# Optimization experiments

Measured on AMD Instinct MI355X. Metric: run time of the kernel, lower is better.

## Reference

```python
import jax, jax.numpy as jnp
import numpy as np

B, N, S = 4, 4096, 1024
C1, C2, CO, K = 128, 256, 128, 16
BN_EPS = 1e-5


def setup_inputs() -> dict:
    key = jax.random.key(0)
    ks = jax.random.split(key, 8)
    s = 0.05
    return {
        "xyz1": jax.random.normal(ks[0], (B, N, 3), jnp.float32),
        "xyz2": jax.random.normal(ks[1], (B, S, 3), jnp.float32),
        "points1": jax.random.normal(ks[2], (B, C1, N), jnp.float32),
        "points2": jax.random.normal(ks[3], (B, C2, S), jnp.float32),
        # fuse = ConvBNReLU1D(384 -> 128, k=1)
        "fuse_w": jax.random.normal(ks[4], (CO, C1 + C2), jnp.float32) * s,
        "fuse_b": jnp.zeros((CO,), jnp.float32),
        "fuse_gamma": jnp.ones((CO,), jnp.float32),
        "fuse_beta": jnp.zeros((CO,), jnp.float32),
        # LaplacianUnit conv1x1 (128 -> 128) + BN
        "lu_w": jax.random.normal(ks[5], (CO, CO), jnp.float32) * s,
        "lu_b": jnp.zeros((CO,), jnp.float32),
        "lu_gamma": jnp.ones((CO,), jnp.float32),
        "lu_beta": jnp.zeros((CO,), jnp.float32),
    }


def _sqdist(a, b):
    # a: [B,N,3], b: [B,M,3] -> [B,N,M] squared euclidean distance
    return ((a * a).sum(-1)[:, :, None] + (b * b).sum(-1)[:, None, :]
            - 2.0 * jnp.einsum("bnc,bmc->bnm", a, b))


def _batchnorm1d(x, gamma, beta):
    # x: [B,C,N], training-mode BN (batch statistics, biased variance)
    mean = x.mean(axis=(0, 2), keepdims=True)
    var = ((x - mean) ** 2).mean(axis=(0, 2), keepdims=True)
    xn = (x - mean) * jax.lax.rsqrt(var + BN_EPS)
    return xn * gamma[None, :, None] + beta[None, :, None]


def _gather_points(pts, idx):
    # pts: [B,M,C], idx: [B,N,k] int -> [B,N,k,C]
    return jax.vmap(lambda p, i: p[i])(pts, idx)


def _forward(xyz1, xyz2, points1, points2,
             fuse_w, fuse_b, fuse_gamma, fuse_beta,
             lu_w, lu_b, lu_gamma, lu_beta):
    p2 = jnp.swapaxes(points2, 1, 2)  # [B,S,C2]
    # --- 3-point interpolation (note: torch code uses topk default largest=True) ---
    dists = _sqdist(xyz1, xyz2)                    # [B,N,S]
    top_d, idx = jax.lax.top_k(dists, 3)           # largest, descending (faithful)
    dist_recip = 1.0 / (top_d + 1e-8)
    weight = dist_recip / dist_recip.sum(axis=2, keepdims=True)  # [B,N,3]
    interp = (_gather_points(p2, idx) * weight[..., None]).sum(axis=2)  # [B,N,C2]
    # --- concat skip + fuse conv1x1 + BN + ReLU ---
    new_pts = jnp.concatenate([jnp.swapaxes(points1, 1, 2), interp], axis=-1)  # [B,N,C1+C2]
    x = jnp.einsum("oc,bnc->bon", fuse_w, new_pts) + fuse_b[None, :, None]     # [B,CO,N]
    x = jax.nn.relu(_batchnorm1d(x, fuse_gamma, fuse_beta))
    # --- LaplacianUnit: KNN(k=16) neighbor-sum minus self ---
    d_self = _sqdist(xyz1, xyz1)                   # [B,N,N]
    _, knn_idx = jax.lax.top_k(-d_self, K)         # k smallest distances -> [B,N,K]
    xt = jnp.swapaxes(x, 1, 2)                     # [B,N,CO]
    nbr_sum = _gather_points(xt, knn_idx).sum(axis=2)  # [B,N,CO]
    dx = jnp.swapaxes(nbr_sum, 1, 2) - x           # [B,CO,N]
    h = jnp.einsum("oc,bcn->bon", lu_w, dx) + lu_b[None, :, None]
    h = _batchnorm1d(jax.nn.relu(h), lu_gamma, lu_beta)  # bn(relu(conv(dx))), faithful order
    return x + h


def reference(xyz1, xyz2, points1, points2,
              fuse_w, fuse_b, fuse_gamma, fuse_beta,
              lu_w, lu_b, lu_gamma, lu_beta):
    return _forward(xyz1, xyz2, points1, points2,
                    fuse_w, fuse_b, fuse_gamma, fuse_beta,
                    lu_w, lu_b, lu_gamma, lu_beta)
```

## Files before the change

kernel.cpp:

```cpp
#include <hip/hip_runtime.h>
#include <cfloat>

#define NB 4
#define NN 4096
#define NS 1024
#define NC1 128
#define NC2 256
#define NCO 128
#define NCC 384
#define NK 16
#define KCHUNK 2048
#define KCAP 160
#define KPAD 161


__device__ __forceinline__ float norm3_np(float x, float y, float z) {
  return __fadd_rn(__fadd_rn(__fmul_rn(x, x), __fmul_rn(y, y)), __fmul_rn(z, z));
}

__device__ __forceinline__ float sqdist_np(float nq, float ns,
                                           float qx, float qy, float qz,
                                           float sx, float sy, float sz) {
  float dot = __fadd_rn(__fadd_rn(__fmul_rn(qx, sx), __fmul_rn(qy, sy)),
                        __fmul_rn(qz, sz));
  return __fsub_rn(__fadd_rn(nq, ns), __fmul_rn(2.0f, dot));
}

__global__ void transpose_k(const float* __restrict__ in, float* __restrict__ out,
                            int rows_in, int cols_in, long in_bs, long out_bs, int out_rs) {
  __shared__ float tile[32][33];
  const int b = blockIdx.z;
  const int c0 = blockIdx.x * 32, r0 = blockIdx.y * 32;
  const float* ib = in + (long)b * in_bs;
  float* ob = out + (long)b * out_bs;
#pragma unroll
  for (int k = 0; k < 32; k += 8) {
    tile[threadIdx.y + k][threadIdx.x] =
        ib[(long)(r0 + threadIdx.y + k) * cols_in + c0 + threadIdx.x];
  }
  __syncthreads();
#pragma unroll
  for (int k = 0; k < 32; k += 8) {
    ob[(long)(c0 + threadIdx.y + k) * out_rs + (r0 + threadIdx.x)] =
        tile[threadIdx.x][threadIdx.y + k];
  }
}

__global__ __launch_bounds__(256) void interp_top3_k(const float* __restrict__ xyz1,
                                                     const float* __restrict__ xyz2,
                                                     float* __restrict__ wW,
                                                     int* __restrict__ wIdx) {
  __shared__ float sx[NS], sy[NS], sz[NS], sn[NS];
  __shared__ float md[256 * 3];
  __shared__ int mi[256 * 3];
  const int b = blockIdx.y;
  const int tid = threadIdx.x;
  for (int i = tid; i < NS; i += 256) {
    long base = ((long)b * NS + i) * 3;
    float x = xyz2[base], y = xyz2[base + 1], z = xyz2[base + 2];
    sx[i] = x; sy[i] = y; sz[i] = z;
    sn[i] = norm3_np(x, y, z);
  }
  __syncthreads();
  const int q = (blockIdx.x << 5) + (tid >> 3);
  const int lane = tid & 7;
  long qb = ((long)b * NN + q) * 3;
  const float qx = xyz1[qb], qy = xyz1[qb + 1], qz = xyz1[qb + 2];
  const float nq = norm3_np(qx, qy, qz);
  float bd[3] = {-FLT_MAX, -FLT_MAX, -FLT_MAX};
  int bi[3] = {0x7fffffff, 0x7fffffff, 0x7fffffff};
  for (int s = lane; s < NS; s += 8) {
    float d = sqdist_np(nq, sn[s], qx, qy, qz, sx[s], sy[s], sz[s]);
    float cd = d; int ci = s;
#pragma unroll
    for (int j = 0; j < 3; ++j) {
      bool gt = cd > bd[j];
      float f = fmaxf(cd, bd[j]);
      float bk = fminf(cd, bd[j]);
      int fi = gt ? ci : bi[j];
      int ki = gt ? bi[j] : ci;
      bd[j] = f; bi[j] = fi; cd = bk; ci = ki;
    }
  }
#pragma unroll
  for (int j = 0; j < 3; ++j) { md[tid * 3 + j] = bd[j]; mi[tid * 3 + j] = bi[j]; }
  __syncthreads();
  if (lane == 0) {
    int p0 = 0, p1 = 0, p2 = 0, p3 = 0, p4 = 0, p5 = 0, p6 = 0, p7 = 0;
    float od[3]; int oi[3];
#pragma unroll
    for (int j = 0; j < 3; ++j) {
      float bv = -FLT_MAX; int bidx = 0x7fffffff; int bl = 0;
#define ITOP_CAND(l, pl)                                                     \
      {                                                                      \
        float t = (pl < 3) ? md[(tid + l) * 3 + pl] : -FLT_MAX;              \
        int ti = (pl < 3) ? mi[(tid + l) * 3 + pl] : 0x7fffffff;             \
        if (t > bv || (t == bv && ti < bidx)) { bv = t; bidx = ti; bl = l; } \
      }
      ITOP_CAND(0, p0) ITOP_CAND(1, p1) ITOP_CAND(2, p2) ITOP_CAND(3, p3)
      ITOP_CAND(4, p4) ITOP_CAND(5, p5) ITOP_CAND(6, p6) ITOP_CAND(7, p7)
#undef ITOP_CAND
      od[j] = bv; oi[j] = bidx;
      p0 += (bl == 0); p1 += (bl == 1); p2 += (bl == 2); p3 += (bl == 3);
      p4 += (bl == 4); p5 += (bl == 5); p6 += (bl == 6); p7 += (bl == 7);
    }
    float r0 = 1.f / (od[0] + 1e-8f);
    float r1 = 1.f / (od[1] + 1e-8f);
    float r2 = 1.f / (od[2] + 1e-8f);
    float sR = __fadd_rn(__fadd_rn(r0, r1), r2);
    long obase = ((long)b * NN + q) * 3;
    wW[obase + 0] = r0 / sR; wW[obase + 1] = r1 / sR; wW[obase + 2] = r2 / sR;
    wIdx[obase + 0] = oi[0]; wIdx[obase + 1] = oi[1]; wIdx[obase + 2] = oi[2];
  }
}

__global__ __launch_bounds__(256) void interp_fill_k(const float* __restrict__ p2t,
                                                     const float* __restrict__ wW,
                                                     const int* __restrict__ wIdx,
                                                     float* __restrict__ nt) {
  const int q = (blockIdx.x << 1) + (threadIdx.x >> 7);
  const int co = threadIdx.x & 127;
  const int b = q >> 12;
  long wb = (long)q * 3;
  float w0 = wW[wb], w1 = wW[wb + 1], w2 = wW[wb + 2];
  int i0 = wIdx[wb], i1 = wIdx[wb + 1], i2 = wIdx[wb + 2];
  const float* r0 = p2t + ((long)(b << 10) + i0) * NC2;
  const float* r1 = p2t + ((long)(b << 10) + i1) * NC2;
  const float* r2 = p2t + ((long)(b << 10) + i2) * NC2;
  float* orow = nt + (long)q * NCC + NC1;
#pragma unroll
  for (int h = 0; h < 2; ++h) {
    int c = co + 128 * h;
    orow[c] = w0 * r0[c] + w1 * r1[c] + w2 * r2[c];
  }
}

template <int C>
__global__ __launch_bounds__(256) void gemm_bias_k(const float* __restrict__ feat,
                                                   const float* __restrict__ W,
                                                   const float* __restrict__ bias,
                                                   float* __restrict__ out) {
  __shared__ float fL[64][36];
  __shared__ float wL[64][36];
  const int r0 = blockIdx.x * 64;
  const int ob = blockIdx.y * 64;
  const int tid = threadIdx.x;
  const int tn = tid & 15;
  const int to = tid >> 4;
  float acc[4][4];
#pragma unroll
  for (int i = 0; i < 4; ++i)
#pragma unroll
    for (int j = 0; j < 4; ++j) acc[i][j] = 0.f;

  for (int c0 = 0; c0 < C; c0 += 32) {
#pragma unroll
    for (int k = 0; k < 8; ++k) {
      int e = tid + 256 * k;
      int rr = e >> 5, cc = e & 31;
      fL[rr][cc] = feat[(long)(r0 + rr) * C + c0 + cc];
    }
#pragma unroll
    for (int k = 0; k < 8; ++k) {
      int e = tid + 256 * k;
      int rr = e >> 5, cc = e & 31;
      wL[rr][cc] = W[(long)(ob + rr) * C + c0 + cc];
    }
    __syncthreads();
#pragma unroll
    for (int cc4 = 0; cc4 < 32; cc4 += 4) {
      float4 fv[4], wv[4];
#pragma unroll
      for (int i = 0; i < 4; ++i) fv[i] = *(const float4*)&fL[tn + 16 * i][cc4];
#pragma unroll
      for (int j = 0; j < 4; ++j) wv[j] = *(const float4*)&wL[to + 16 * j][cc4];
#pragma unroll
      for (int i = 0; i < 4; ++i)
#pragma unroll
        for (int j = 0; j < 4; ++j) {
          acc[i][j] += fv[i].x * wv[j].x + fv[i].y * wv[j].y +
                       fv[i].z * wv[j].z + fv[i].w * wv[j].w;
        }
    }
    __syncthreads();
  }
  const int b = r0 >> 12;
  const int n0 = r0 & 4095;
#pragma unroll
  for (int i = 0; i < 4; ++i) {
    int n = n0 + tn + 16 * i;
#pragma unroll
    for (int j = 0; j < 4; ++j) {
      int o = ob + to + 16 * j;
      out[((long)(b * NCO + o) << 12) + n] = acc[i][j] + bias[o];
    }
  }
}

__global__ __launch_bounds__(256) void bn_stats_k(const float* __restrict__ v,
                                                  const float* __restrict__ gamma,
                                                  const float* __restrict__ beta,
                                                  float* __restrict__ stats, int relu_in) {
  __shared__ float rs[256], rq[256];
  const int o = blockIdx.x, tid = threadIdx.x;
  float s = 0.f, ss = 0.f;
  for (int i = tid; i < NB * NN; i += 256) {
    int b = i >> 12, n = i & 4095;
    float val = v[(((long)b * NCO + o) << 12) + n];
    if (relu_in) val = fmaxf(val, 0.f);
    s += val;
    ss += val * val;
  }
  rs[tid] = s; rq[tid] = ss;
  __syncthreads();
  for (int off = 128; off > 0; off >>= 1) {
    if (tid < off) { rs[tid] += rs[tid + off]; rq[tid] += rq[tid + off]; }
    __syncthreads();
  }
  if (tid == 0) {
    float m = rs[0] * (1.f / 16384.f);
    float var = rq[0] * (1.f / 16384.f) - m * m;
    var = fmaxf(var, 0.f);
    float inv = rsqrtf(var + 1e-5f);
    stats[o] = m;
    stats[128 + o] = inv * gamma[o];
    stats[256 + o] = beta[o];
  }
}

__global__ void fuse_apply_k(const float* __restrict__ xp, const float* __restrict__ stats,
                             float* __restrict__ x, float* __restrict__ xt) {
  const int stride = gridDim.x * blockDim.x;
  for (int idx = blockIdx.x * blockDim.x + threadIdx.x; idx < NB * NCO * NN; idx += stride) {
    int o = (idx >> 12) & 127;
    int b = idx >> 19;
    int n = idx & 4095;
    float v = (xp[idx] - stats[o]) * stats[128 + o] + stats[256 + o];
    v = fmaxf(v, 0.f);
    x[idx] = v;
    xt[(((long)b << 12) + n) * NCO + o] = v;
  }
}

__global__ __launch_bounds__(256) void knn_k(const float* __restrict__ xyz1,
                                             int* __restrict__ knn) {
  __shared__ float4 sc[KCHUNK];
  __shared__ float bufd[32][KPAD];
  __shared__ int bufi[32][KPAD];
  const int b = blockIdx.y;
  const int tid = threadIdx.x;
  const int ql = tid >> 3;
  const int q = (blockIdx.x << 5) + ql;
  const int lane = tid & 7;
  const int gb = (tid & 63) - lane;
  const long qb = ((long)b * NN + q) * 3;
  const float qx = xyz1[qb], qy = xyz1[qb + 1], qz = xyz1[qb + 2];
  const float nq = norm3_np(qx, qy, qz);

  float a0 = FLT_MAX, a1 = FLT_MAX, c0 = FLT_MAX, c1 = FLT_MAX;
  for (int ch = 0; ch < 2; ++ch) {
    for (int i = tid; i < KCHUNK; i += 256) {
      long base = ((long)b * NN + ch * KCHUNK + i) * 3;
      float x = xyz1[base], y = xyz1[base + 1], z = xyz1[base + 2];
      sc[i] = make_float4(x, y, z, norm3_np(x, y, z));
    }
    __syncthreads();
#pragma unroll 2
    for (int i = lane; i < KCHUNK; i += 16) {
      float4 ca = sc[i];
      float4 cb = sc[i + 8];
      float da = sqdist_np(nq, ca.w, qx, qy, qz, ca.x, ca.y, ca.z);
      float db = sqdist_np(nq, cb.w, qx, qy, qz, cb.x, cb.y, cb.z);
      float ha = fmaxf(da, a0); a0 = fminf(da, a0); a1 = fminf(ha, a1);
      float hb = fmaxf(db, c0); c0 = fminf(db, c0); c1 = fminf(hb, c1);
    }
    __syncthreads();
  }
  float tau = fminf(fmaxf(a0, c0), fminf(a1, c1));
  tau = fmaxf(tau, __shfl_xor(tau, 1, 64));
  tau = fmaxf(tau, __shfl_xor(tau, 2, 64));
  tau = fmaxf(tau, __shfl_xor(tau, 4, 64));

  int mycnt = 0;
  for (int ch = 0; ch < 2; ++ch) {
    for (int i = tid; i < KCHUNK; i += 256) {
      long base = ((long)b * NN + ch * KCHUNK + i) * 3;
      float x = xyz1[base], y = xyz1[base + 1], z = xyz1[base + 2];
      sc[i] = make_float4(x, y, z, norm3_np(x, y, z));
    }
    __syncthreads();
    const int cb = ch * KCHUNK;
    for (int i = lane; i < KCHUNK; i += 16) {
      float4 v0 = sc[i];
      float4 v1 = sc[i + 8];
      float d0 = sqdist_np(nq, v0.w, qx, qy, qz, v0.x, v0.y, v0.z);
      float d1 = sqdist_np(nq, v1.w, qx, qy, qz, v1.x, v1.y, v1.z);
      bool s0 = (d0 <= tau);
      bool s1 = (d1 <= tau);
      unsigned long long m0 = __ballot(s0);
      unsigned long long m1 = __ballot(s1);
      unsigned g0 = (unsigned)((m0 >> gb) & 0xFFull);
      unsigned g1 = (unsigned)((m1 >> gb) & 0xFFull);
      if (s0) {
        int pos = mycnt + __popc(g0 & ((1u << lane) - 1u));
        if (pos < KCAP) { bufd[ql][pos] = d0; bufi[ql][pos] = cb + i; }
      }
      if (s1) {
        int pos = mycnt + __popc(g0) + __popc(g1 & ((1u << lane) - 1u));
        if (pos < KCAP) { bufd[ql][pos] = d1; bufi[ql][pos] = cb + i + 8; }
      }
      mycnt += __popc(g0) + __popc(g1);
    }
    __syncthreads();
  }

  float bd[NK]; int bi[NK];
#pragma unroll
  for (int j = 0; j < NK; ++j) { bd[j] = FLT_MAX; bi[j] = 0x7fffffff; }
  if (mycnt > KCAP) {
    for (int s = lane; s < NN; s += 8) {
      long base = ((long)b * NN + s) * 3;
      float x = xyz1[base], y = xyz1[base + 1], z = xyz1[base + 2];
      float d = sqdist_np(nq, norm3_np(x, y, z), qx, qy, qz, x, y, z);
      if (d <= tau) {
        float cd = d; int ci = s;
#pragma unroll
        for (int j = 0; j < NK; ++j) {
          bool lt = cd < bd[j];
          float dmin = fminf(cd, bd[j]);
          float dmax = fmaxf(cd, bd[j]);
          int imin = lt ? ci : bi[j];
          int imax = lt ? bi[j] : ci;
          bd[j] = dmin; bi[j] = imin; cd = dmax; ci = imax;
        }
      }
    }
  } else {
    for (int j0 = lane; j0 < mycnt; j0 += 8) {
      float cd = bufd[ql][j0]; int ci = bufi[ql][j0];
#pragma unroll
      for (int j = 0; j < NK; ++j) {
        bool lt = (cd < bd[j]) || (cd == bd[j] && ci < bi[j]);
        float nd = lt ? cd : bd[j];
        float xd = lt ? bd[j] : cd;
        int ni = lt ? ci : bi[j];
        int xi = lt ? bi[j] : ci;
        bd[j] = nd; bi[j] = ni; cd = xd; ci = xi;
      }
    }
  }
  __syncthreads();

  float* md = (float*)sc;
  int* mi = (int*)sc + 4096;
#pragma unroll
  for (int j = 0; j < NK; ++j) { md[tid * NK + j] = bd[j]; mi[tid * NK + j] = bi[j]; }
  __syncthreads();
  if (lane == 0) {
    int p0 = 0, p1 = 0, p2 = 0, p3 = 0, p4 = 0, p5 = 0, p6 = 0, p7 = 0;
    long obase = ((long)b * NN + q) * NK;
    for (int j = 0; j < NK; ++j) {
      float bv = FLT_MAX; int bidx = 0x7fffffff; int bl = 0;
#define KNN_CAND(l, pl)                                                      \
      {                                                                      \
        float t = (pl < NK) ? md[(tid + l) * NK + pl] : FLT_MAX;             \
        int ti = (pl < NK) ? mi[(tid + l) * NK + pl] : 0x7fffffff;           \
        if (t < bv || (t == bv && ti < bidx)) { bv = t; bidx = ti; bl = l; } \
      }
      KNN_CAND(0, p0) KNN_CAND(1, p1) KNN_CAND(2, p2) KNN_CAND(3, p3)
      KNN_CAND(4, p4) KNN_CAND(5, p5) KNN_CAND(6, p6) KNN_CAND(7, p7)
#undef KNN_CAND
      knn[obase + j] = bidx;
      p0 += (bl == 0); p1 += (bl == 1); p2 += (bl == 2); p3 += (bl == 3);
      p4 += (bl == 4); p5 += (bl == 5); p6 += (bl == 6); p7 += (bl == 7);
    }
  }
}

__global__ __launch_bounds__(256) void lap_gather_k(const float* __restrict__ xt,
                                                    const int* __restrict__ knn,
                                                    float* __restrict__ dxt) {
  const int q = (blockIdx.x << 1) + (threadIdx.x >> 7);
  const int o = threadIdx.x & 127;
  const int b = q >> 12;
  const int* kid = knn + (long)q * NK;
  const long bb = ((long)b << 12) * NCO;
  float s = 0.f;
#pragma unroll
  for (int k = 0; k < NK; ++k) {
    int m = kid[k];
    s += xt[bb + (long)m * NCO + o];
  }
  dxt[(long)q * NCO + o] = s - xt[(long)q * NCO + o];
}

__global__ void final_k(const float* __restrict__ x, const float* __restrict__ hp,
                        const float* __restrict__ stats, float* __restrict__ out) {
  const int stride = gridDim.x * blockDim.x;
  for (int idx = blockIdx.x * blockDim.x + threadIdx.x; idx < NB * NCO * NN; idx += stride) {
    int o = (idx >> 12) & 127;
    float r = fmaxf(hp[idx], 0.f);
    out[idx] = x[idx] + (r - stats[o]) * stats[128 + o] + stats[256 + o];
  }
}

extern "C" void kernel_launch(void* const* d_in, const int* in_sizes, int n_in,
                              void* d_out, int out_size, void* d_ws, size_t ws_size,
                              hipStream_t stream) {
  const float* xyz1 = (const float*)d_in[0];
  const float* xyz2 = (const float*)d_in[1];
  const float* points1 = (const float*)d_in[2];
  const float* points2 = (const float*)d_in[3];
  const float* fuse_w = (const float*)d_in[4];
  const float* fuse_b = (const float*)d_in[5];
  const float* fuse_g = (const float*)d_in[6];
  const float* fuse_be = (const float*)d_in[7];
  const float* lu_w = (const float*)d_in[8];
  const float* lu_b = (const float*)d_in[9];
  const float* lu_g = (const float*)d_in[10];
  const float* lu_be = (const float*)d_in[11];
  (void)in_sizes; (void)n_in; (void)out_size; (void)ws_size;

  char* ws = (char*)d_ws;
  float* p2t = (float*)(ws);
  float* wW = (float*)(ws + 4194304);
  int* wIdx = (int*)(ws + 4390912);
  float* st1 = (float*)(ws + 4587520);
  float* st2 = (float*)(ws + 4589056);
  int* knn = (int*)(ws + 4590592);
  float* nt = (float*)(ws + 5639168);
  float* xp = (float*)(ws + 30804992);
  float* x = (float*)(ws + 39193600);
  float* xt = nt;
  float* dxt = nt + 2097152;
  float* hp = nt + 4194304;

  dim3 tb(32, 8);
  transpose_k<<<dim3(32, 8, NB), tb, 0, stream>>>(points2, p2t, 256, 1024, 262144L, 262144L, 256);
  transpose_k<<<dim3(128, 4, NB), tb, 0, stream>>>(points1, nt, 128, 4096, 524288L, 1572864L, 384);
  interp_top3_k<<<dim3(128, NB), 256, 0, stream>>>(xyz1, xyz2, wW, wIdx);
  interp_fill_k<<<8192, 256, 0, stream>>>(p2t, wW, wIdx, nt);
  gemm_bias_k<NCC><<<dim3(256, 2), 256, 0, stream>>>(nt, fuse_w, fuse_b, xp);
  bn_stats_k<<<128, 256, 0, stream>>>(xp, fuse_g, fuse_be, st1, 0);
  fuse_apply_k<<<2048, 256, 0, stream>>>(xp, st1, x, xt);
  knn_k<<<dim3(128, NB), 256, 0, stream>>>(xyz1, knn);
  lap_gather_k<<<8192, 256, 0, stream>>>(xt, knn, dxt);
  gemm_bias_k<NCO><<<dim3(256, 2), 256, 0, stream>>>(dxt, lu_w, lu_b, hp);
  bn_stats_k<<<128, 256, 0, stream>>>(hp, lu_g, lu_be, st2, 1);
  final_k<<<2048, 256, 0, stream>>>(x, hp, st2, (float*)d_out);
}
```

Baseline: 262.4 us.

## Tile fuse_apply transpose via shared memory, widen KNN loops, skip top3 inserts

```diff
diff --git a/kernel.cpp b/kernel.cpp
--- a/kernel.cpp
+++ b/kernel.cpp
@@ -71,15 +71,17 @@
   int bi[3] = {0x7fffffff, 0x7fffffff, 0x7fffffff};
   for (int s = lane; s < NS; s += 8) {
     float d = sqdist_np(nq, sn[s], qx, qy, qz, sx[s], sy[s], sz[s]);
-    float cd = d; int ci = s;
-#pragma unroll
-    for (int j = 0; j < 3; ++j) {
-      bool gt = cd > bd[j];
-      float f = fmaxf(cd, bd[j]);
-      float bk = fminf(cd, bd[j]);
-      int fi = gt ? ci : bi[j];
-      int ki = gt ? bi[j] : ci;
-      bd[j] = f; bi[j] = fi; cd = bk; ci = ki;
+    if (d > bd[2]) {
+      float cd = d; int ci = s;
+#pragma unroll
+      for (int j = 0; j < 3; ++j) {
+        bool gt = cd > bd[j];
+        float f = fmaxf(cd, bd[j]);
+        float bk = fminf(cd, bd[j]);
+        int fi = gt ? ci : bi[j];
+        int ki = gt ? bi[j] : ci;
+        bd[j] = f; bi[j] = fi; cd = bk; ci = ki;
+      }
     }
   }
 #pragma unroll
@@ -230,15 +232,25 @@
 
 __global__ void fuse_apply_k(const float* __restrict__ xp, const float* __restrict__ stats,
                              float* __restrict__ x, float* __restrict__ xt) {
-  const int stride = gridDim.x * blockDim.x;
-  for (int idx = blockIdx.x * blockDim.x + threadIdx.x; idx < NB * NCO * NN; idx += stride) {
-    int o = (idx >> 12) & 127;
-    int b = idx >> 19;
-    int n = idx & 4095;
+  __shared__ float tile[32][33];
+  const int b = blockIdx.z;
+  const int n0 = blockIdx.x * 32;
+  const int o0 = blockIdx.y * 32;
+  const int tx = threadIdx.x, ty = threadIdx.y;
+#pragma unroll
+  for (int k = 0; k < 32; k += 8) {
+    int o = o0 + ty + k;
+    long idx = (((long)b * NCO + o) << 12) + n0 + tx;
     float v = (xp[idx] - stats[o]) * stats[128 + o] + stats[256 + o];
     v = fmaxf(v, 0.f);
     x[idx] = v;
-    xt[(((long)b << 12) + n) * NCO + o] = v;
+    tile[ty + k][tx] = v;
+  }
+  __syncthreads();
+#pragma unroll
+  for (int k = 0; k < 32; k += 8) {
+    int n = n0 + ty + k;
+    xt[((long)(b << 12) + n) * NCO + o0 + tx] = tile[tx][ty + k];
   }
 }
 
@@ -257,7 +269,8 @@
   const float qx = xyz1[qb], qy = xyz1[qb + 1], qz = xyz1[qb + 2];
   const float nq = norm3_np(qx, qy, qz);
 
-  float a0 = FLT_MAX, a1 = FLT_MAX, c0 = FLT_MAX, c1 = FLT_MAX;
+  float ta0 = FLT_MAX, ta1 = FLT_MAX, tb0 = FLT_MAX, tb1 = FLT_MAX;
+  float tc0 = FLT_MAX, tc1 = FLT_MAX, td0 = FLT_MAX, td1 = FLT_MAX;
   for (int ch = 0; ch < 2; ++ch) {
     for (int i = tid; i < KCHUNK; i += 256) {
       long base = ((long)b * NN + ch * KCHUNK + i) * 3;
@@ -265,18 +278,25 @@
       sc[i] = make_float4(x, y, z, norm3_np(x, y, z));
     }
     __syncthreads();
-#pragma unroll 2
-    for (int i = lane; i < KCHUNK; i += 16) {
-      float4 ca = sc[i];
-      float4 cb = sc[i + 8];
-      float da = sqdist_np(nq, ca.w, qx, qy, qz, ca.x, ca.y, ca.z);
-      float db = sqdist_np(nq, cb.w, qx, qy, qz, cb.x, cb.y, cb.z);
-      float ha = fmaxf(da, a0); a0 = fminf(da, a0); a1 = fminf(ha, a1);
-      float hb = fmaxf(db, c0); c0 = fminf(db, c0); c1 = fminf(hb, c1);
-    }
-    __syncthreads();
-  }
-  float tau = fminf(fmaxf(a0, c0), fminf(a1, c1));
+    for (int i = lane; i < KCHUNK; i += 32) {
+      float4 v0 = sc[i], v1 = sc[i + 8], v2 = sc[i + 16], v3 = sc[i + 24];
+      float d0 = sqdist_np(nq, v0.w, qx, qy, qz, v0.x, v0.y, v0.z);
+      float d1 = sqdist_np(nq, v1.w, qx, qy, qz, v1.x, v1.y, v1.z);
+      float d2 = sqdist_np(nq, v2.w, qx, qy, qz, v2.x, v2.y, v2.z);
+      float d3 = sqdist_np(nq, v3.w, qx, qy, qz, v3.x, v3.y, v3.z);
+      float h0 = fmaxf(d0, ta0); ta0 = fminf(d0, ta0); ta1 = fminf(h0, ta1);
+      float h1 = fmaxf(d1, tb0); tb0 = fminf(d1, tb0); tb1 = fminf(h1, tb1);
+      float h2 = fmaxf(d2, tc0); tc0 = fminf(d2, tc0); tc1 = fminf(h2, tc1);
+      float h3 = fmaxf(d3, td0); td0 = fminf(d3, td0); td1 = fminf(h3, td1);
+    }
+    __syncthreads();
+  }
+  float m1 = fminf(fminf(ta0, tb0), fminf(tc0, td0));
+  float s0 = (ta0 == m1) ? ta1 : ta0;
+  float s1 = (tb0 == m1) ? tb1 : tb0;
+  float s2 = (tc0 == m1) ? tc1 : tc0;
+  float s3 = (td0 == m1) ? td1 : td0;
+  float tau = fminf(fminf(s0, s1), fminf(s2, s3));
   tau = fmaxf(tau, __shfl_xor(tau, 1, 64));
   tau = fmaxf(tau, __shfl_xor(tau, 2, 64));
   tau = fmaxf(tau, __shfl_xor(tau, 4, 64));
@@ -290,26 +310,40 @@
     }
     __syncthreads();
     const int cb = ch * KCHUNK;
-    for (int i = lane; i < KCHUNK; i += 16) {
-      float4 v0 = sc[i];
-      float4 v1 = sc[i + 8];
+    for (int i = lane; i < KCHUNK; i += 32) {
+      float4 v0 = sc[i], v1 = sc[i + 8], v2 = sc[i + 16], v3 = sc[i + 24];
       float d0 = sqdist_np(nq, v0.w, qx, qy, qz, v0.x, v0.y, v0.z);
       float d1 = sqdist_np(nq, v1.w, qx, qy, qz, v1.x, v1.y, v1.z);
-      bool s0 = (d0 <= tau);
-      bool s1 = (d1 <= tau);
-      unsigned long long m0 = __ballot(s0);
-      unsigned long long m1 = __ballot(s1);
+      float d2 = sqdist_np(nq, v2.w, qx, qy, qz, v2.x, v2.y, v2.z);
+      float d3 = sqdist_np(nq, v3.w, qx, qy, qz, v3.x, v3.y, v3.z);
+      bool sv0 = (d0 <= tau), sv1 = (d1 <= tau), sv2 = (d2 <= tau), sv3 = (d3 <= tau);
+      unsigned long long m0 = __ballot(sv0);
+      unsigned long long m1b = __ballot(sv1);
+      unsigned long long m2 = __ballot(sv2);
+      unsigned long long m3 = __ballot(sv3);
       unsigned g0 = (unsigned)((m0 >> gb) & 0xFFull);
-      unsigned g1 = (unsigned)((m1 >> gb) & 0xFFull);
-      if (s0) {
-        int pos = mycnt + __popc(g0 & ((1u << lane) - 1u));
+      unsigned g1 = (unsigned)((m1b >> gb) & 0xFFull);
+      unsigned g2 = (unsigned)((m2 >> gb) & 0xFFull);
+      unsigned g3 = (unsigned)((m3 >> gb) & 0xFFull);
+      unsigned below = (1u << lane) - 1u;
+      int c0p = __popc(g0), c1p = __popc(g1), c2p = __popc(g2);
+      if (sv0) {
+        int pos = mycnt + __popc(g0 & below);
         if (pos < KCAP) { bufd[ql][pos] = d0; bufi[ql][pos] = cb + i; }
       }
-      if (s1) {
-        int pos = mycnt + __popc(g0) + __popc(g1 & ((1u << lane) - 1u));
+      if (sv1) {
+        int pos = mycnt + c0p + __popc(g1 & below);
         if (pos < KCAP) { bufd[ql][pos] = d1; bufi[ql][pos] = cb + i + 8; }
       }
-      mycnt += __popc(g0) + __popc(g1);
+      if (sv2) {
+        int pos = mycnt + c0p + c1p + __popc(g2 & below);
+        if (pos < KCAP) { bufd[ql][pos] = d2; bufi[ql][pos] = cb + i + 16; }
+      }
+      if (sv3) {
+        int pos = mycnt + c0p + c1p + c2p + __popc(g3 & below);
+        if (pos < KCAP) { bufd[ql][pos] = d3; bufi[ql][pos] = cb + i + 24; }
+      }
+      mycnt += c0p + c1p + c2p + __popc(g3);
     }
     __syncthreads();
   }
@@ -442,7 +476,7 @@
   interp_fill_k<<<8192, 256, 0, stream>>>(p2t, wW, wIdx, nt);
   gemm_bias_k<NCC><<<dim3(256, 2), 256, 0, stream>>>(nt, fuse_w, fuse_b, xp);
   bn_stats_k<<<128, 256, 0, stream>>>(xp, fuse_g, fuse_be, st1, 0);
-  fuse_apply_k<<<2048, 256, 0, stream>>>(xp, st1, x, xt);
+  fuse_apply_k<<<dim3(128, 4, NB), tb, 0, stream>>>(xp, st1, x, xt);
   knn_k<<<dim3(128, NB), 256, 0, stream>>>(xyz1, knn);
   lap_gather_k<<<8192, 256, 0, stream>>>(xt, knn, dxt);
   gemm_bias_k<NCO><<<dim3(256, 2), 256, 0, stream>>>(dxt, lu_w, lu_b, hp);
```

New measurement: 258.6 us, median of 3. Within noise of the previous version (-1.5%).
